# Performance work log

Measured on AMD Instinct MI355X. Metric: run time of the kernel, lower is better.

Reference implementation:

```python
import jax, jax.numpy as jnp
import numpy as np

B, S, D_MODEL, D_HIDDEN = 4, 2048, 1024, 4096

# --- BitNet b1.58-style quantizers (STE in bwd version) ---

def act_quant(x):
    # per-token int8 absmax quantization over last dim
    scale = 127.0 / jnp.clip(jnp.max(jnp.abs(x), axis=-1, keepdims=True), 1e-5)
    return jnp.clip(jnp.round(x * scale), -128, 127) / scale

def weight_quant(w):
    # ternary weights with global mean-abs scale
    scale = 1.0 / jnp.clip(jnp.mean(jnp.abs(w)), 1e-5)
    return jnp.clip(jnp.round(w * scale), -1, 1) / scale

def bit_linear(x, w):
    # STE: forward uses quantized values, gradient passes through
    xq = x + jax.lax.stop_gradient(act_quant(x) - x)
    wq = w + jax.lax.stop_gradient(weight_quant(w) - w)
    return jnp.einsum('bsd,hd->bsh', xq, wq)

def depthwise_conv1d(x_bcl, w, b):
    # x_bcl: [B, C, L], w: [C, 1, 3], b: [C]
    y = jax.lax.conv_general_dilated(
        x_bcl, w, window_strides=(1,), padding=[(1, 1)],
        dimension_numbers=('NCH', 'OIH', 'NCH'),
        feature_group_count=x_bcl.shape[1])
    return y + b[None, :, None]


def setup_inputs() -> dict:
    key = jax.random.key(0)
    ks = jax.random.split(key, 5)
    lim1 = 1.0 / np.sqrt(D_MODEL)
    lim2 = 1.0 / np.sqrt(D_HIDDEN)
    limc = 1.0 / np.sqrt(3.0)  # fan_in = 1*3 for depthwise conv
    return {
        'x': jax.random.normal(ks[0], (B, S, D_MODEL), dtype=jnp.float32),
        'w1': jax.random.uniform(ks[1], (D_HIDDEN, D_MODEL), jnp.float32, -lim1, lim1),
        'conv_w': jax.random.uniform(ks[2], (D_HIDDEN, 1, 3), jnp.float32, -limc, limc),
        'conv_b': jax.random.uniform(ks[3], (D_HIDDEN,), jnp.float32, -limc, limc),
        'w2': jax.random.uniform(ks[4], (D_MODEL, D_HIDDEN), jnp.float32, -lim2, lim2),
    }


def reference(x, w1, conv_w, conv_b, w2):
    h = bit_linear(x, w1)                      # [B, S, H]
    h = depthwise_conv1d(h.transpose(0, 2, 1), conv_w, conv_b)  # [B, H, S]
    h = h.transpose(0, 2, 1)                   # [B, S, H]
    h = jax.nn.silu(h)
    return bit_linear(h, w2)                   # [B, S, D]
```

## Files before the change

### kernel.cpp

```cpp
#include <hip/hip_runtime.h>
#include <cstdint>

#define S_    2048
#define DM    1024
#define DH    4096
#define NTOK  8192
#define WELEM 4194304
#define CT    8
#define NS    3

typedef int v4i __attribute__((ext_vector_type(4)));

#define GLOAD_LDS16(g, l)                                                   \
    __builtin_amdgcn_global_load_lds(                                       \
        (const __attribute__((address_space(1))) void*)(g),                 \
        (__attribute__((address_space(3))) void*)(l), 16, 0, 0)

#define WAITCNT_VM16 0x4F70
#define WAITCNT_VM0  0x0F70

__global__ __launch_bounds__(256) void absmean_partial(const float4* __restrict__ wa,
                                                       const float4* __restrict__ wb,
                                                       double* __restrict__ partial) {
    __shared__ double red[256];
    const float4* w = (blockIdx.x < 1024) ? wa : wb;
    int base = (blockIdx.x & 1023) * 1024;
    double s = 0.0;
#pragma unroll
    for (int k = 0; k < 4; ++k) {
        float4 v = w[base + (k << 8) + threadIdx.x];
        s += (double)fabsf(v.x) + (double)fabsf(v.y) +
             (double)fabsf(v.z) + (double)fabsf(v.w);
    }
    red[threadIdx.x] = s;
    __syncthreads();
    for (int off = 128; off > 0; off >>= 1) {
        if (threadIdx.x < off) red[threadIdx.x] += red[threadIdx.x + off];
        __syncthreads();
    }
    if (threadIdx.x == 0) partial[blockIdx.x] = red[0];
}

__global__ __launch_bounds__(256) void finalize_scales(const double* __restrict__ part,
                                                       float* __restrict__ sc) {
    __shared__ double red[1024];
#pragma unroll 1
    for (int m = 0; m < 2; ++m) {
        const double* p = part + m * 1024;
        __syncthreads();
#pragma unroll
        for (int k = 0; k < 4; ++k) red[(k << 8) + threadIdx.x] = p[(k << 8) + threadIdx.x];
        __syncthreads();
        double s = red[threadIdx.x] + red[threadIdx.x + 256] +
                   red[threadIdx.x + 512] + red[threadIdx.x + 768];
        __syncthreads();
        red[threadIdx.x] = s;
        __syncthreads();
        for (int off = 128; off > 0; off >>= 1) {
            if (threadIdx.x < off) red[threadIdx.x] += red[threadIdx.x + off];
            __syncthreads();
        }
        if (threadIdx.x == 0) {
            double mean = red[0] / (double)WELEM;
            float mf = fmaxf((float)mean, 1e-5f);
            float scale = 1.0f / mf;
            sc[2 * m]     = scale;
            sc[2 * m + 1] = 1.0f / scale;
        }
    }
}

__global__ __launch_bounds__(256) void quant_w(const float4* __restrict__ wa,
                                               const float4* __restrict__ wb,
                                               char4* __restrict__ qa,
                                               char4* __restrict__ qb,
                                               const float* __restrict__ sc) {
    bool second = blockIdx.x >= 4096;
    const float4* w = second ? wb : wa;
    char4* q = second ? qb : qa;
    float scale = sc[second ? 2 : 0];
    int i = (blockIdx.x & 4095) * 256 + threadIdx.x;
    float4 v = w[i];
    char4 o;
    o.x = (signed char)(int)fminf(fmaxf(rintf(v.x * scale), -1.f), 1.f);
    o.y = (signed char)(int)fminf(fmaxf(rintf(v.y * scale), -1.f), 1.f);
    o.z = (signed char)(int)fminf(fmaxf(rintf(v.z * scale), -1.f), 1.f);
    o.w = (signed char)(int)fminf(fmaxf(rintf(v.w * scale), -1.f), 1.f);
    q[i] = o;
}

__global__ __launch_bounds__(256) void quant_x_kernel(const float4* __restrict__ x,
                                                      char4* __restrict__ q,
                                                      float* __restrict__ dq) {
    __shared__ float red[256];
    int t = blockIdx.x;
    float4 v = x[(size_t)t * 256 + threadIdx.x];
    float mx = fmaxf(fmaxf(fabsf(v.x), fabsf(v.y)), fmaxf(fabsf(v.z), fabsf(v.w)));
    red[threadIdx.x] = mx;
    __syncthreads();
    for (int off = 128; off > 0; off >>= 1) {
        if (threadIdx.x < off) red[threadIdx.x] = fmaxf(red[threadIdx.x], red[threadIdx.x + off]);
        __syncthreads();
    }
    float scale = 127.0f / fmaxf(red[0], 1e-5f);
    char4 o;
    o.x = (signed char)(int)fminf(fmaxf(rintf(v.x * scale), -128.f), 127.f);
    o.y = (signed char)(int)fminf(fmaxf(rintf(v.y * scale), -128.f), 127.f);
    o.z = (signed char)(int)fminf(fmaxf(rintf(v.z * scale), -128.f), 127.f);
    o.w = (signed char)(int)fminf(fmaxf(rintf(v.w * scale), -128.f), 127.f);
    q[(size_t)t * 256 + threadIdx.x] = o;
    if (threadIdx.x == 0) dq[t] = 1.0f / scale;
}

__global__ __launch_bounds__(512) void conv_silu_quant(const float4* __restrict__ h,
                                                       const float4* __restrict__ cw,
                                                       const float4* __restrict__ cb,
                                                       char4* __restrict__ q,
                                                       float* __restrict__ dq) {
    __shared__ float red[2][8];
    const int tid = threadIdx.x;
    const int t0 = blockIdx.x * CT;
    const int s0 = t0 & (S_ - 1);

    float4 w0[2], w1[2], w2[2], bb[2];
#pragma unroll
    for (int k = 0; k < 2; ++k) {
        int g = (k << 9) + tid;
        w0[k] = cw[3 * g]; w1[k] = cw[3 * g + 1]; w2[k] = cw[3 * g + 2];
        bb[k] = cb[g];
    }

    const float4 z4 = {0.f, 0.f, 0.f, 0.f};
    float4 pv[2], cu[2], nx[2], pf[2];
#pragma unroll
    for (int k = 0; k < 2; ++k) {
        int g = (k << 9) + tid;
        pv[k] = (s0 > 0) ? h[(size_t)(t0 - 1) * 1024 + g] : z4;
        cu[k] = h[(size_t)t0 * 1024 + g];
        nx[k] = h[(size_t)(t0 + 1) * 1024 + g];
    }

#pragma unroll
    for (int i = 0; i < CT; ++i) {
        const int t = t0 + i;
        bool hp2 = (s0 + i + 2) < S_;
#pragma unroll
        for (int k = 0; k < 2; ++k)
            pf[k] = hp2 ? h[(size_t)(t + 2) * 1024 + (k << 9) + tid] : z4;

        float4 v[2];
        float mx = 0.f;
#pragma unroll
        for (int k = 0; k < 2; ++k) {
            float4 a = pv[k], b = cu[k], c = nx[k];
            float4 y;
            y.x = w0[k].x * a.x + w0[k].y * b.x + w0[k].z * c.x + bb[k].x;
            y.y = w0[k].w * a.y + w1[k].x * b.y + w1[k].y * c.y + bb[k].y;
            y.z = w1[k].z * a.z + w1[k].w * b.z + w2[k].x * c.z + bb[k].z;
            y.w = w2[k].y * a.w + w2[k].z * b.w + w2[k].w * c.w + bb[k].w;
            float4 r;
            r.x = y.x / (1.0f + expf(-y.x));
            r.y = y.y / (1.0f + expf(-y.y));
            r.z = y.z / (1.0f + expf(-y.z));
            r.w = y.w / (1.0f + expf(-y.w));
            v[k] = r;
            mx = fmaxf(mx, fmaxf(fmaxf(fabsf(r.x), fabsf(r.y)), fmaxf(fabsf(r.z), fabsf(r.w))));
        }
#pragma unroll
        for (int off = 32; off > 0; off >>= 1)
            mx = fmaxf(mx, __shfl_down(mx, off, 64));
        if ((tid & 63) == 0) red[i & 1][tid >> 6] = mx;
        __syncthreads();
        float rmax = red[i & 1][0];
#pragma unroll
        for (int w = 1; w < 8; ++w) rmax = fmaxf(rmax, red[i & 1][w]);
        float scale = 127.0f / fmaxf(rmax, 1e-5f);
#pragma unroll
        for (int k = 0; k < 2; ++k) {
            char4 o;
            o.x = (signed char)(int)fminf(fmaxf(rintf(v[k].x * scale), -128.f), 127.f);
            o.y = (signed char)(int)fminf(fmaxf(rintf(v[k].y * scale), -128.f), 127.f);
            o.z = (signed char)(int)fminf(fmaxf(rintf(v[k].z * scale), -128.f), 127.f);
            o.w = (signed char)(int)fminf(fmaxf(rintf(v[k].w * scale), -128.f), 127.f);
            q[(size_t)t * 1024 + (k << 9) + tid] = o;
        }
        if (tid == 0) dq[t] = 1.0f / scale;
#pragma unroll
        for (int k = 0; k < 2; ++k) { pv[k] = cu[k]; cu[k] = nx[k]; nx[k] = pf[k]; }
    }
}

__global__ __launch_bounds__(320) void gemm_i8_pc(const int8_t* __restrict__ A,
                                                  const int8_t* __restrict__ Bm,
                                                  float* __restrict__ C,
                                                  const float* __restrict__ rowdq,
                                                  const float* __restrict__ sc, int slot,
                                                  int N, int K) {
    __shared__ __align__(16) int8_t Alds[NS][8192];
    __shared__ __align__(16) int8_t Blds[NS][8192];
    __shared__ int flag[NS];
    __shared__ int cnt[NS];
    const int tid  = threadIdx.x;
    const int lane = tid & 63;
    const int wave = tid >> 6;
    const int mbase = blockIdx.y << 7;
    const int nbase = blockIdx.x << 7;
    const int niter = K >> 6;

    if (tid < NS) { flag[tid] = 0; cnt[tid] = 0; }
    __syncthreads();

    if (wave == 4) {
        const int r_l = lane >> 2;
        const int c_l = ((lane & 3) - ((lane >> 3) & 3)) & 3;
        const int8_t* Agb = A  + (size_t)(mbase + r_l) * K + c_l * 16;
        const int8_t* Bgb = Bm + (size_t)(nbase + r_l) * K + c_l * 16;
        const size_t ts = (size_t)16 * K;

        auto issue = [&](int j) {
            const int s = j % NS;
            const int k0 = j << 6;
#pragma unroll
            for (int t = 0; t < 8; ++t)
                GLOAD_LDS16(Agb + (size_t)t * ts + k0, &Alds[s][t << 10]);
#pragma unroll
            for (int t = 0; t < 8; ++t)
                GLOAD_LDS16(Bgb + (size_t)t * ts + k0, &Blds[s][t << 10]);
        };

        issue(0);
        if (niter > 1) issue(1);
        for (int it = 0; it < niter; ++it) {
            if (it + 1 < niter) __builtin_amdgcn_s_waitcnt(WAITCNT_VM16);
            else                __builtin_amdgcn_s_waitcnt(WAITCNT_VM0);
            __hip_atomic_store(&flag[it % NS], it + 1,
                               __ATOMIC_RELEASE, __HIP_MEMORY_SCOPE_WORKGROUP);
            const int j = it + 2;
            if (j < niter) {
                const int s = j % NS, need = 4 * (j / NS);
                while (__hip_atomic_load(&cnt[s], __ATOMIC_ACQUIRE,
                                         __HIP_MEMORY_SCOPE_WORKGROUP) < need)
                    __builtin_amdgcn_s_sleep(1);
                issue(j);
            }
        }
        return;
    }

    const int wm4 = (wave >> 1) << 2;
    const int wn4 = (wave & 1) << 2;
    const int m_l = lane & 15, q_l = lane >> 4;
    const int fro = (4 * m_l + ((q_l + (m_l >> 1)) & 3)) << 4;

    v4i acc[4][4] = {};
    for (int it = 0; it < niter; ++it) {
        const int s = it % NS;
        while (__hip_atomic_load(&flag[s], __ATOMIC_ACQUIRE,
                                 __HIP_MEMORY_SCOPE_WORKGROUP) < it + 1)
            __builtin_amdgcn_s_sleep(1);
        v4i af[4], bf[4];
#pragma unroll
        for (int i = 0; i < 4; ++i)
            af[i] = *reinterpret_cast<const v4i*>(&Alds[s][fro + ((wm4 + i) << 10)]);
#pragma unroll
        for (int j = 0; j < 4; ++j)
            bf[j] = *reinterpret_cast<const v4i*>(&Blds[s][fro + ((wn4 + j) << 10)]);
        __hip_atomic_fetch_add(&cnt[s], 1, __ATOMIC_ACQ_REL, __HIP_MEMORY_SCOPE_WORKGROUP);
#pragma unroll
        for (int i = 0; i < 4; ++i)
#pragma unroll
            for (int j = 0; j < 4; ++j)
                acc[i][j] = __builtin_amdgcn_mfma_i32_16x16x64_i8(af[i], bf[j], acc[i][j], 0, 0, 0);
    }

    const float wdq = sc[slot];
    const int quad = lane >> 4;
    const int col  = lane & 15;
#pragma unroll
    for (int i = 0; i < 4; ++i) {
#pragma unroll
        for (int r = 0; r < 4; ++r) {
            int m = mbase + ((wm4 + i) << 4) + (quad << 2) + r;
            float rs = rowdq[m] * wdq;
#pragma unroll
            for (int j = 0; j < 4; ++j) {
                int n = nbase + ((wn4 + j) << 4) + col;
                C[(size_t)m * N + n] = (float)acc[i][j][r] * rs;
            }
        }
    }
}

extern "C" void kernel_launch(void* const* d_in, const int* in_sizes, int n_in,
                              void* d_out, int out_size, void* d_ws, size_t ws_size,
                              hipStream_t stream) {
    const float* x  = (const float*)d_in[0];
    const float* w1 = (const float*)d_in[1];
    const float* cw = (const float*)d_in[2];
    const float* cb = (const float*)d_in[3];
    const float* w2 = (const float*)d_in[4];
    float* out = (float*)d_out;
    char* ws = (char*)d_ws;

    double* part  = (double*)(ws + 0);
    float*  sc    = (float*)(ws + 16384);
    float*  dqx   = (float*)(ws + 16640);
    float*  dqh   = (float*)(ws + 49408);
    int8_t* qw1   = (int8_t*)(ws + 82176);
    int8_t* qw2   = (int8_t*)(ws + 4276480);
    int8_t* qx    = (int8_t*)(ws + 8470784);
    int8_t* qh    = (int8_t*)(ws + 16859392);
    float*  h     = (float*)(ws + 50413824);

    absmean_partial<<<2048, 256, 0, stream>>>((const float4*)w1, (const float4*)w2, part);
    finalize_scales<<<1, 256, 0, stream>>>(part, sc);
    quant_w<<<8192, 256, 0, stream>>>((const float4*)w1, (const float4*)w2,
                                      (char4*)qw1, (char4*)qw2, sc);
    quant_x_kernel<<<NTOK, 256, 0, stream>>>((const float4*)x, (char4*)qx, dqx);

    dim3 g1(DH / 128, NTOK / 128);
    gemm_i8_pc<<<g1, 320, 0, stream>>>(qx, qw1, h, dqx, sc, 1, DH, DM);

    conv_silu_quant<<<NTOK / CT, 512, 0, stream>>>((const float4*)h, (const float4*)cw,
                                                   (const float4*)cb, (char4*)qh, dqh);

    dim3 g2(DM / 128, NTOK / 128);
    gemm_i8_pc<<<g2, 320, 0, stream>>>(qh, qw2, out, dqh, sc, 3, DM, DH);
}
```

Measured before the change: 281.8 us.

## Store intermediate hidden in fp16, fuse quant kernels, relax GEMM pipeline atomics

The first GEMM now writes its hidden activation as fp16 instead of fp32, halving the intermediate write and the conv/SiLU read traffic. The conv kernel is reworked to process 8 contiguous channels per thread and emit 8-byte int8 stores. The weight and activation quantization kernels are merged into one launch. The producer/consumer atomics in the GEMM pipeline use relaxed ordering with an explicit LDS waitcnt, and only one lane per wave increments the counter. fp16 storage of the hidden state may perturb the per-token absmax quantization slightly, and the relaxed ordering relies on the waitcnt for correctness.

```diff
diff --git a/kernel.cpp b/kernel.cpp
--- a/kernel.cpp
+++ b/kernel.cpp
@@ -10,14 +10,17 @@
 #define NS    3
 
 typedef int v4i __attribute__((ext_vector_type(4)));
+typedef _Float16 half8 __attribute__((ext_vector_type(8)));
+typedef char char8v __attribute__((ext_vector_type(8)));
 
 #define GLOAD_LDS16(g, l)                                                   \
     __builtin_amdgcn_global_load_lds(                                       \
         (const __attribute__((address_space(1))) void*)(g),                 \
         (__attribute__((address_space(3))) void*)(l), 16, 0, 0)
 
-#define WAITCNT_VM16 0x4F70
-#define WAITCNT_VM0  0x0F70
+#define WAITCNT_VM16  0x4F70
+#define WAITCNT_VM0   0x0F70
+#define WAITCNT_LGKM0 0xC07F
 
 __global__ __launch_bounds__(256) void absmean_partial(const float4* __restrict__ wa,
                                                        const float4* __restrict__ wb,
@@ -70,101 +73,100 @@
     }
 }
 
-__global__ __launch_bounds__(256) void quant_w(const float4* __restrict__ wa,
-                                               const float4* __restrict__ wb,
-                                               char4* __restrict__ qa,
-                                               char4* __restrict__ qb,
-                                               const float* __restrict__ sc) {
-    bool second = blockIdx.x >= 4096;
-    const float4* w = second ? wb : wa;
-    char4* q = second ? qb : qa;
-    float scale = sc[second ? 2 : 0];
-    int i = (blockIdx.x & 4095) * 256 + threadIdx.x;
-    float4 v = w[i];
-    char4 o;
-    o.x = (signed char)(int)fminf(fmaxf(rintf(v.x * scale), -1.f), 1.f);
-    o.y = (signed char)(int)fminf(fmaxf(rintf(v.y * scale), -1.f), 1.f);
-    o.z = (signed char)(int)fminf(fmaxf(rintf(v.z * scale), -1.f), 1.f);
-    o.w = (signed char)(int)fminf(fmaxf(rintf(v.w * scale), -1.f), 1.f);
-    q[i] = o;
-}
-
-__global__ __launch_bounds__(256) void quant_x_kernel(const float4* __restrict__ x,
-                                                      char4* __restrict__ q,
-                                                      float* __restrict__ dq) {
+__global__ __launch_bounds__(256) void quant_all(const float4* __restrict__ w1,
+                                                 const float4* __restrict__ w2,
+                                                 const float4* __restrict__ x,
+                                                 char4* __restrict__ qw1,
+                                                 char4* __restrict__ qw2,
+                                                 char4* __restrict__ qx,
+                                                 float* __restrict__ dqx,
+                                                 const float* __restrict__ sc) {
     __shared__ float red[256];
-    int t = blockIdx.x;
-    float4 v = x[(size_t)t * 256 + threadIdx.x];
-    float mx = fmaxf(fmaxf(fabsf(v.x), fabsf(v.y)), fmaxf(fabsf(v.z), fabsf(v.w)));
-    red[threadIdx.x] = mx;
-    __syncthreads();
-    for (int off = 128; off > 0; off >>= 1) {
-        if (threadIdx.x < off) red[threadIdx.x] = fmaxf(red[threadIdx.x], red[threadIdx.x + off]);
-        __syncthreads();
-    }
-    float scale = 127.0f / fmaxf(red[0], 1e-5f);
-    char4 o;
-    o.x = (signed char)(int)fminf(fmaxf(rintf(v.x * scale), -128.f), 127.f);
-    o.y = (signed char)(int)fminf(fmaxf(rintf(v.y * scale), -128.f), 127.f);
-    o.z = (signed char)(int)fminf(fmaxf(rintf(v.z * scale), -128.f), 127.f);
-    o.w = (signed char)(int)fminf(fmaxf(rintf(v.w * scale), -128.f), 127.f);
-    q[(size_t)t * 256 + threadIdx.x] = o;
-    if (threadIdx.x == 0) dq[t] = 1.0f / scale;
-}
-
-__global__ __launch_bounds__(512) void conv_silu_quant(const float4* __restrict__ h,
-                                                       const float4* __restrict__ cw,
-                                                       const float4* __restrict__ cb,
-                                                       char4* __restrict__ q,
+    if (blockIdx.x < 8192) {
+        bool second = blockIdx.x >= 4096;
+        const float4* w = second ? w2 : w1;
+        char4* q = second ? qw2 : qw1;
+        float scale = sc[second ? 2 : 0];
+        int i = (blockIdx.x & 4095) * 256 + threadIdx.x;
+        float4 v = w[i];
+        char4 o;
+        o.x = (signed char)(int)fminf(fmaxf(rintf(v.x * scale), -1.f), 1.f);
+        o.y = (signed char)(int)fminf(fmaxf(rintf(v.y * scale), -1.f), 1.f);
+        o.z = (signed char)(int)fminf(fmaxf(rintf(v.z * scale), -1.f), 1.f);
+        o.w = (signed char)(int)fminf(fmaxf(rintf(v.w * scale), -1.f), 1.f);
+        q[i] = o;
+    } else {
+        int t = blockIdx.x - 8192;
+        float4 v = x[(size_t)t * 256 + threadIdx.x];
+        float mx = fmaxf(fmaxf(fabsf(v.x), fabsf(v.y)), fmaxf(fabsf(v.z), fabsf(v.w)));
+        red[threadIdx.x] = mx;
+        __syncthreads();
+        for (int off = 128; off > 0; off >>= 1) {
+            if (threadIdx.x < off) red[threadIdx.x] = fmaxf(red[threadIdx.x], red[threadIdx.x + off]);
+            __syncthreads();
+        }
+        float scale = 127.0f / fmaxf(red[0], 1e-5f);
+        char4 o;
+        o.x = (signed char)(int)fminf(fmaxf(rintf(v.x * scale), -128.f), 127.f);
+        o.y = (signed char)(int)fminf(fmaxf(rintf(v.y * scale), -128.f), 127.f);
+        o.z = (signed char)(int)fminf(fmaxf(rintf(v.z * scale), -128.f), 127.f);
+        o.w = (signed char)(int)fminf(fmaxf(rintf(v.w * scale), -128.f), 127.f);
+        qx[(size_t)t * 256 + threadIdx.x] = o;
+        if (threadIdx.x == 0) dqx[t] = 1.0f / scale;
+    }
+}
+
+__global__ __launch_bounds__(512) void conv_silu_quant(const half8* __restrict__ h,
+                                                       const float4* __restrict__ cwv,
+                                                       const float4* __restrict__ cbv,
+                                                       char8v* __restrict__ q,
                                                        float* __restrict__ dq) {
     __shared__ float red[2][8];
     const int tid = threadIdx.x;
     const int t0 = blockIdx.x * CT;
     const int s0 = t0 & (S_ - 1);
 
-    float4 w0[2], w1[2], w2[2], bb[2];
-#pragma unroll
-    for (int k = 0; k < 2; ++k) {
-        int g = (k << 9) + tid;
-        w0[k] = cw[3 * g]; w1[k] = cw[3 * g + 1]; w2[k] = cw[3 * g + 2];
-        bb[k] = cb[g];
-    }
-
-    const float4 z4 = {0.f, 0.f, 0.f, 0.f};
-    float4 pv[2], cu[2], nx[2], pf[2];
-#pragma unroll
-    for (int k = 0; k < 2; ++k) {
-        int g = (k << 9) + tid;
-        pv[k] = (s0 > 0) ? h[(size_t)(t0 - 1) * 1024 + g] : z4;
-        cu[k] = h[(size_t)t0 * 1024 + g];
-        nx[k] = h[(size_t)(t0 + 1) * 1024 + g];
-    }
+    float wc[24], bs[8];
+    {
+        float4 tmp;
+#pragma unroll
+        for (int i = 0; i < 6; ++i) {
+            tmp = cwv[tid * 6 + i];
+            wc[4 * i] = tmp.x; wc[4 * i + 1] = tmp.y; wc[4 * i + 2] = tmp.z; wc[4 * i + 3] = tmp.w;
+        }
+        tmp = cbv[tid * 2];     bs[0] = tmp.x; bs[1] = tmp.y; bs[2] = tmp.z; bs[3] = tmp.w;
+        tmp = cbv[tid * 2 + 1]; bs[4] = tmp.x; bs[5] = tmp.y; bs[6] = tmp.z; bs[7] = tmp.w;
+    }
+
+    auto ldrow = [&](int t, bool valid, float* dst) {
+        if (valid) {
+            half8 raw = h[(size_t)t * 512 + tid];
+#pragma unroll
+            for (int e = 0; e < 8; ++e) dst[e] = (float)raw[e];
+        } else {
+#pragma unroll
+            for (int e = 0; e < 8; ++e) dst[e] = 0.f;
+        }
+    };
+
+    float pv[8], cu[8], nx[8], pf[8];
+    ldrow(t0 - 1, s0 > 0, pv);
+    ldrow(t0, true, cu);
+    ldrow(t0 + 1, true, nx);
 
 #pragma unroll
     for (int i = 0; i < CT; ++i) {
         const int t = t0 + i;
-        bool hp2 = (s0 + i + 2) < S_;
-#pragma unroll
-        for (int k = 0; k < 2; ++k)
-            pf[k] = hp2 ? h[(size_t)(t + 2) * 1024 + (k << 9) + tid] : z4;
-
-        float4 v[2];
+        ldrow(t + 2, (s0 + i + 2) < S_, pf);
+
+        float v[8];
         float mx = 0.f;
 #pragma unroll
-        for (int k = 0; k < 2; ++k) {
-            float4 a = pv[k], b = cu[k], c = nx[k];
-            float4 y;
-            y.x = w0[k].x * a.x + w0[k].y * b.x + w0[k].z * c.x + bb[k].x;
-            y.y = w0[k].w * a.y + w1[k].x * b.y + w1[k].y * c.y + bb[k].y;
-            y.z = w1[k].z * a.z + w1[k].w * b.z + w2[k].x * c.z + bb[k].z;
-            y.w = w2[k].y * a.w + w2[k].z * b.w + w2[k].w * c.w + bb[k].w;
-            float4 r;
-            r.x = y.x / (1.0f + expf(-y.x));
-            r.y = y.y / (1.0f + expf(-y.y));
-            r.z = y.z / (1.0f + expf(-y.z));
-            r.w = y.w / (1.0f + expf(-y.w));
-            v[k] = r;
-            mx = fmaxf(mx, fmaxf(fmaxf(fabsf(r.x), fabsf(r.y)), fmaxf(fabsf(r.z), fabsf(r.w))));
+        for (int e = 0; e < 8; ++e) {
+            float y = wc[3 * e] * pv[e] + wc[3 * e + 1] * cu[e] + wc[3 * e + 2] * nx[e] + bs[e];
+            float r = y / (1.0f + expf(-y));
+            v[e] = r;
+            mx = fmaxf(mx, fabsf(r));
         }
 #pragma unroll
         for (int off = 32; off > 0; off >>= 1)
@@ -175,24 +177,21 @@
 #pragma unroll
         for (int w = 1; w < 8; ++w) rmax = fmaxf(rmax, red[i & 1][w]);
         float scale = 127.0f / fmaxf(rmax, 1e-5f);
-#pragma unroll
-        for (int k = 0; k < 2; ++k) {
-            char4 o;
-            o.x = (signed char)(int)fminf(fmaxf(rintf(v[k].x * scale), -128.f), 127.f);
-            o.y = (signed char)(int)fminf(fmaxf(rintf(v[k].y * scale), -128.f), 127.f);
-            o.z = (signed char)(int)fminf(fmaxf(rintf(v[k].z * scale), -128.f), 127.f);
-            o.w = (signed char)(int)fminf(fmaxf(rintf(v[k].w * scale), -128.f), 127.f);
-            q[(size_t)t * 1024 + (k << 9) + tid] = o;
-        }
+        char8v o;
+#pragma unroll
+        for (int e = 0; e < 8; ++e)
+            o[e] = (signed char)(int)fminf(fmaxf(rintf(v[e] * scale), -128.f), 127.f);
+        q[(size_t)t * 512 + tid] = o;
         if (tid == 0) dq[t] = 1.0f / scale;
 #pragma unroll
-        for (int k = 0; k < 2; ++k) { pv[k] = cu[k]; cu[k] = nx[k]; nx[k] = pf[k]; }
-    }
-}
-
+        for (int e = 0; e < 8; ++e) { pv[e] = cu[e]; cu[e] = nx[e]; nx[e] = pf[e]; }
+    }
+}
+
+template <typename OutT>
 __global__ __launch_bounds__(320) void gemm_i8_pc(const int8_t* __restrict__ A,
                                                   const int8_t* __restrict__ Bm,
-                                                  float* __restrict__ C,
+                                                  OutT* __restrict__ C,
                                                   const float* __restrict__ rowdq,
                                                   const float* __restrict__ sc, int slot,
                                                   int N, int K) {
@@ -234,11 +233,11 @@
             if (it + 1 < niter) __builtin_amdgcn_s_waitcnt(WAITCNT_VM16);
             else                __builtin_amdgcn_s_waitcnt(WAITCNT_VM0);
             __hip_atomic_store(&flag[it % NS], it + 1,
-                               __ATOMIC_RELEASE, __HIP_MEMORY_SCOPE_WORKGROUP);
+                               __ATOMIC_RELAXED, __HIP_MEMORY_SCOPE_WORKGROUP);
             const int j = it + 2;
             if (j < niter) {
-                const int s = j % NS, need = 4 * (j / NS);
-                while (__hip_atomic_load(&cnt[s], __ATOMIC_ACQUIRE,
+                const int s2 = j % NS, need = 4 * (j / NS);
+                while (__hip_atomic_load(&cnt[s2], __ATOMIC_RELAXED,
                                          __HIP_MEMORY_SCOPE_WORKGROUP) < need)
                     __builtin_amdgcn_s_sleep(1);
                 issue(j);
@@ -265,7 +264,10 @@
 #pragma unroll
         for (int j = 0; j < 4; ++j)
             bf[j] = *reinterpret_cast<const v4i*>(&Blds[s][fro + ((wn4 + j) << 10)]);
-        __hip_atomic_fetch_add(&cnt[s], 1, __ATOMIC_ACQ_REL, __HIP_MEMORY_SCOPE_WORKGROUP);
+        __builtin_amdgcn_s_waitcnt(WAITCNT_LGKM0);
+        if (lane == 0)
+            __hip_atomic_fetch_add(&cnt[s], 1, __ATOMIC_RELAXED,
+                                   __HIP_MEMORY_SCOPE_WORKGROUP);
 #pragma unroll
         for (int i = 0; i < 4; ++i)
 #pragma unroll
@@ -285,7 +287,7 @@
 #pragma unroll
             for (int j = 0; j < 4; ++j) {
                 int n = nbase + ((wn4 + j) << 4) + col;
-                C[(size_t)m * N + n] = (float)acc[i][j][r] * rs;
+                C[(size_t)m * N + n] = (OutT)((float)acc[i][j][r] * rs);
             }
         }
     }
@@ -310,20 +312,20 @@
     int8_t* qw2   = (int8_t*)(ws + 4276480);
     int8_t* qx    = (int8_t*)(ws + 8470784);
     int8_t* qh    = (int8_t*)(ws + 16859392);
-    float*  h     = (float*)(ws + 50413824);
+    _Float16* h   = (_Float16*)(ws + 50413824);
 
     absmean_partial<<<2048, 256, 0, stream>>>((const float4*)w1, (const float4*)w2, part);
     finalize_scales<<<1, 256, 0, stream>>>(part, sc);
-    quant_w<<<8192, 256, 0, stream>>>((const float4*)w1, (const float4*)w2,
-                                      (char4*)qw1, (char4*)qw2, sc);
-    quant_x_kernel<<<NTOK, 256, 0, stream>>>((const float4*)x, (char4*)qx, dqx);
+    quant_all<<<16384, 256, 0, stream>>>((const float4*)w1, (const float4*)w2,
+                                         (const float4*)x, (char4*)qw1, (char4*)qw2,
+                                         (char4*)qx, dqx, sc);
 
     dim3 g1(DH / 128, NTOK / 128);
-    gemm_i8_pc<<<g1, 320, 0, stream>>>(qx, qw1, h, dqx, sc, 1, DH, DM);
-
-    conv_silu_quant<<<NTOK / CT, 512, 0, stream>>>((const float4*)h, (const float4*)cw,
-                                                   (const float4*)cb, (char4*)qh, dqh);
+    gemm_i8_pc<_Float16><<<g1, 320, 0, stream>>>(qx, qw1, h, dqx, sc, 1, DH, DM);
+
+    conv_silu_quant<<<NTOK / CT, 512, 0, stream>>>((const half8*)h, (const float4*)cw,
+                                                   (const float4*)cb, (char8v*)qh, dqh);
 
     dim3 g2(DM / 128, NTOK / 128);
-    gemm_i8_pc<<<g2, 320, 0, stream>>>(qh, qw2, out, dqh, sc, 3, DM, DH);
-}
+    gemm_i8_pc<float><<<g2, 320, 0, stream>>>(qh, qw2, out, dqh, sc, 3, DM, DH);
+}
```

Result: faster. 273.5 us (-3.0%).
